# Kernel optimization log

Measured on AMD Instinct MI355X. Metric: run time of the kernel, lower is better.

The kernel has to match this reference:

```python
import jax, jax.numpy as jnp
import numpy as np

N_NODES = 50000
N_EDGES = 320000
D_IN = 256
D_OUT = 256


def setup_inputs() -> dict:
    key = jax.random.key(0)
    k1, k2, k3, k4, k5, k6, k7 = jax.random.split(key, 7)
    s = 1.0 / np.sqrt(D_IN)
    return {
        "node_features": jax.random.normal(k1, (N_NODES, D_IN), dtype=jnp.float32),
        "edge_index": jax.random.randint(k2, (2, N_EDGES), 0, N_NODES, dtype=jnp.int64),
        "w1": jax.random.uniform(k3, (D_OUT, D_IN), jnp.float32, -s, s),
        "w2": jax.random.uniform(k4, (D_OUT, D_IN), jnp.float32, -s, s),
        "w3": jax.random.uniform(k5, (D_OUT, D_IN), jnp.float32, -s, s),
        "b3": jax.random.uniform(k6, (D_OUT,), jnp.float32, -s, s),
    }


def reference(node_features, edge_index, w1, w2, w3, b3):
    # GraphSAGE-style conv: project, gather messages from senders,
    # scatter-sum at receivers, project, combine with self term.
    n = node_features.shape[0]
    proj = node_features @ w3.T + b3                 # [N, D_OUT]
    msgs = proj[edge_index[0]]                       # [E, D_OUT] gather senders
    agg = jax.ops.segment_sum(msgs, edge_index[1], num_segments=n)  # [N, D_OUT]
    out = node_features @ w1.T + agg @ w2.T          # [N, D_OUT]
    return out
```

## Files before the change

kernel.cpp:

```cpp
#include <hip/hip_runtime.h>

#define NN 50000
#define NPAD 50048
#define NE 320000
#define D 256
#define CAP 64
#define NCONV 6250

typedef __bf16 bf16x8 __attribute__((ext_vector_type(8)));
typedef float f32x4 __attribute__((ext_vector_type(4)));

__device__ __forceinline__ unsigned short f2bf(float f) {
    unsigned u = __builtin_bit_cast(unsigned, f);
    unsigned r = u + 0x7FFFu + ((u >> 16) & 1u);
    return (unsigned short)(r >> 16);
}
__device__ __forceinline__ float bflo(unsigned u) {
    return __builtin_bit_cast(float, u << 16);
}
__device__ __forceinline__ float bfhi(unsigned u) {
    return __builtin_bit_cast(float, u & 0xFFFF0000u);
}
__device__ __forceinline__ unsigned packbf(float lo, float hi) {
    return (unsigned)f2bf(lo) | ((unsigned)f2bf(hi) << 16);
}

__global__ __launch_bounds__(256) void prep_weights(
        const float* __restrict__ w1, const float* __restrict__ w2,
        const float* __restrict__ w3, const float* __restrict__ b3,
        unsigned short* __restrict__ WTT, float* __restrict__ bvec,
        int* __restrict__ cnt) {
    const int j = blockIdx.x;
    const int k = threadIdx.x;
    const int g = j * 256 + k;
    if (g < NN) cnt[g] = 0;
    __shared__ float w2row[D];
    __shared__ float red[D];
    w2row[k] = w2[j * D + k];
    __syncthreads();
    float acc = 0.f;
    #pragma unroll 8
    for (int o = 0; o < D; ++o) acc += w2row[o] * w3[o * D + k];
    WTT[(size_t)j * 512 + k]     = f2bf(w1[j * D + k]);
    WTT[(size_t)j * 512 + D + k] = f2bf(acc);
    red[k] = w2row[k] * b3[k];
    __syncthreads();
    for (int s = 128; s > 0; s >>= 1) {
        if (k < s) red[k] += red[k + s];
        __syncthreads();
    }
    if (k == 0) bvec[j] = red[0];
}

__global__ __launch_bounds__(256) void convert_and_csr(
        const float* __restrict__ x, unsigned short* __restrict__ xbf,
        const int* __restrict__ ei, int* __restrict__ csr, int* __restrict__ cnt) {
    const int b = blockIdx.x;
    if (b < NCONV) {
        const size_t i = ((size_t)b * 256 + threadIdx.x) * 8;
        const float4 a0 = *reinterpret_cast<const float4*>(x + i);
        const float4 a1 = *reinterpret_cast<const float4*>(x + i + 4);
        ushort4 o0 = {f2bf(a0.x), f2bf(a0.y), f2bf(a0.z), f2bf(a0.w)};
        ushort4 o1 = {f2bf(a1.x), f2bf(a1.y), f2bf(a1.z), f2bf(a1.w)};
        *reinterpret_cast<ushort4*>(xbf + i)     = o0;
        *reinterpret_cast<ushort4*>(xbf + i + 4) = o1;
    } else {
        const int e = (b - NCONV) * 256 + threadIdx.x;
        if (e < NE) {
            const int src = ei[e];
            const int dst = ei[NE + e];
            const int pos = atomicAdd(cnt + dst, 1);
            if (pos < CAP) csr[(size_t)dst * CAP + pos] = src;
        }
    }
}

__global__ __launch_bounds__(256) void agg_gather(
        const unsigned short* __restrict__ xbf, const int* __restrict__ csr,
        const int* __restrict__ cnt, unsigned short* __restrict__ aggbf) {
    const int node = blockIdx.x * 8 + (threadIdx.x >> 5);
    const int l32  = threadIdx.x & 31;
    if (node >= NN) return;
    int d = cnt[node]; if (d > CAP) d = CAP;
    const int* __restrict__ row = csr + (size_t)node * CAP;
    const int d32 = d < 32 ? d : 32;
    int myidx = 0;
    if (l32 < d32) myidx = row[l32];
    float a0 = 0.f, a1 = 0.f, a2 = 0.f, a3 = 0.f;
    float a4 = 0.f, a5 = 0.f, a6 = 0.f, a7 = 0.f;
    int i = 0;
    for (; i + 4 <= d32; i += 4) {
        const int s0 = __shfl(myidx, i,     32);
        const int s1 = __shfl(myidx, i + 1, 32);
        const int s2 = __shfl(myidx, i + 2, 32);
        const int s3 = __shfl(myidx, i + 3, 32);
        const uint4 p = *reinterpret_cast<const uint4*>(xbf + (size_t)s0 * D + l32 * 8);
        const uint4 q = *reinterpret_cast<const uint4*>(xbf + (size_t)s1 * D + l32 * 8);
        const uint4 u = *reinterpret_cast<const uint4*>(xbf + (size_t)s2 * D + l32 * 8);
        const uint4 v = *reinterpret_cast<const uint4*>(xbf + (size_t)s3 * D + l32 * 8);
        a0 += (bflo(p.x) + bflo(q.x)) + (bflo(u.x) + bflo(v.x));
        a1 += (bfhi(p.x) + bfhi(q.x)) + (bfhi(u.x) + bfhi(v.x));
        a2 += (bflo(p.y) + bflo(q.y)) + (bflo(u.y) + bflo(v.y));
        a3 += (bfhi(p.y) + bfhi(q.y)) + (bfhi(u.y) + bfhi(v.y));
        a4 += (bflo(p.z) + bflo(q.z)) + (bflo(u.z) + bflo(v.z));
        a5 += (bfhi(p.z) + bfhi(q.z)) + (bfhi(u.z) + bfhi(v.z));
        a6 += (bflo(p.w) + bflo(q.w)) + (bflo(u.w) + bflo(v.w));
        a7 += (bfhi(p.w) + bfhi(q.w)) + (bfhi(u.w) + bfhi(v.w));
    }
    for (; i < d32; ++i) {
        const int s = __shfl(myidx, i, 32);
        const uint4 p = *reinterpret_cast<const uint4*>(xbf + (size_t)s * D + l32 * 8);
        a0 += bflo(p.x); a1 += bfhi(p.x);
        a2 += bflo(p.y); a3 += bfhi(p.y);
        a4 += bflo(p.z); a5 += bfhi(p.z);
        a6 += bflo(p.w); a7 += bfhi(p.w);
    }
    for (; i < d; ++i) {
        const uint4 p = *reinterpret_cast<const uint4*>(xbf + (size_t)row[i] * D + l32 * 8);
        a0 += bflo(p.x); a1 += bfhi(p.x);
        a2 += bflo(p.y); a3 += bfhi(p.y);
        a4 += bflo(p.z); a5 += bfhi(p.z);
        a6 += bflo(p.w); a7 += bfhi(p.w);
    }
    uint4 o = {packbf(a0, a1), packbf(a2, a3), packbf(a4, a5), packbf(a6, a7)};
    *reinterpret_cast<uint4*>(aggbf + (size_t)node * D + l32 * 8) = o;
}

__global__ __launch_bounds__(256) void gemm_tiled(
        const unsigned short* __restrict__ xbf, const unsigned short* __restrict__ aggbf,
        const unsigned short* __restrict__ WTT, const float* __restrict__ bvec,
        const int* __restrict__ cnt, float* __restrict__ out) {
    __shared__ __align__(16) unsigned short ldsA[64 * 64];
    __shared__ __align__(16) unsigned short ldsB[128 * 64];

    const int tid  = threadIdx.x;
    const int w    = tid >> 6;
    const int lane = tid & 63;
    const int l16  = lane & 15;
    const int g4   = lane >> 4;
    const int wm   = w >> 1, wn = w & 1;
    const int gr0  = (blockIdx.x >> 1) * 64;
    const int nb0  = (blockIdx.x & 1) * 128;

    f32x4 acc[2][4];
    #pragma unroll
    for (int a = 0; a < 2; ++a)
        #pragma unroll
        for (int b = 0; b < 4; ++b) acc[a][b] = (f32x4)0.f;

    for (int kt = 0; kt < 8; ++kt) {
        if (kt) __syncthreads();
        {
            const unsigned short* __restrict__ srcA = (kt < 4) ? xbf : aggbf;
            const int kcA = (kt & 3) * 64;
            #pragma unroll
            for (int p = 0; p < 2; ++p) {
                const int idx = p * 256 + w * 64 + lane;
                const int r = idx >> 3, c = idx & 7;
                const int sw = (c ^ (r & 7)) << 3;
                const unsigned short* gp = srcA + ((size_t)(gr0 + r) << 8) + kcA + sw;
                unsigned short* lp = &ldsA[(p * 256 + w * 64) << 3];
                __builtin_amdgcn_global_load_lds(
                    (const __attribute__((address_space(1))) void*)(const void*)gp,
                    (__attribute__((address_space(3))) void*)(void*)lp, 16, 0, 0);
            }
            const int kcB = kt * 64;
            #pragma unroll
            for (int p = 0; p < 4; ++p) {
                const int idx = p * 256 + w * 64 + lane;
                const int r = idx >> 3, c = idx & 7;
                const int sw = (c ^ (r & 7)) << 3;
                const unsigned short* gp = WTT + ((size_t)(nb0 + r) << 9) + kcB + sw;
                unsigned short* lp = &ldsB[(p * 256 + w * 64) << 3];
                __builtin_amdgcn_global_load_lds(
                    (const __attribute__((address_space(1))) void*)(const void*)gp,
                    (__attribute__((address_space(3))) void*)(void*)lp, 16, 0, 0);
            }
        }
        __syncthreads();

        #pragma unroll
        for (int kh = 0; kh < 2; ++kh) {
            const int cb = kh * 4 + g4;
            bf16x8 af[2], bfr[4];
            #pragma unroll
            for (int f = 0; f < 2; ++f) {
                const int ra = wm * 32 + f * 16 + l16;
                af[f] = *reinterpret_cast<const bf16x8*>(
                    &ldsA[(ra * 8 + (cb ^ (ra & 7))) * 8]);
            }
            #pragma unroll
            for (int f = 0; f < 4; ++f) {
                const int rb = wn * 64 + f * 16 + l16;
                bfr[f] = *reinterpret_cast<const bf16x8*>(
                    &ldsB[(rb * 8 + (cb ^ (rb & 7))) * 8]);
            }
            #pragma unroll
            for (int fm = 0; fm < 2; ++fm)
                #pragma unroll
                for (int fn = 0; fn < 4; ++fn)
                    acc[fm][fn] = __builtin_amdgcn_mfma_f32_16x16x32_bf16(
                        af[fm], bfr[fn], acc[fm][fn], 0, 0, 0);
        }
    }

    const int col0 = nb0 + wn * 64 + l16;
    float bv[4];
    #pragma unroll
    for (int fn = 0; fn < 4; ++fn) bv[fn] = bvec[col0 + fn * 16];
    #pragma unroll
    for (int fm = 0; fm < 2; ++fm) {
        #pragma unroll
        for (int i = 0; i < 4; ++i) {
            const int row = gr0 + wm * 32 + fm * 16 + g4 * 4 + i;
            if (row < NN) {
                const float dg = (float)cnt[row];
                float* op = out + ((size_t)row << 8) + col0;
                #pragma unroll
                for (int fn = 0; fn < 4; ++fn)
                    op[fn * 16] = acc[fm][fn][i] + dg * bv[fn];
            }
        }
    }
}

extern "C" void kernel_launch(void* const* d_in, const int* in_sizes, int n_in,
                              void* d_out, int out_size, void* d_ws, size_t ws_size,
                              hipStream_t stream) {
    const float* x  = (const float*)d_in[0];
    const int*   ei = (const int*)d_in[1];
    const float* w1 = (const float*)d_in[2];
    const float* w2 = (const float*)d_in[3];
    const float* w3 = (const float*)d_in[4];
    const float* b3 = (const float*)d_in[5];
    float* out = (float*)d_out;

    unsigned short* xbf   = (unsigned short*)d_ws;
    unsigned short* aggbf = xbf + (size_t)NPAD * D;
    unsigned short* WTT   = aggbf + (size_t)NPAD * D;
    float* bvec = (float*)(WTT + (size_t)D * 512);
    int*   cnt  = (int*)(bvec + D);
    int*   csr  = cnt + NN;

    prep_weights<<<D, 256, 0, stream>>>(w1, w2, w3, b3, WTT, bvec, cnt);
    convert_and_csr<<<NCONV + (NE + 255) / 256, 256, 0, stream>>>(x, xbf, ei, csr, cnt);
    agg_gather<<<(NN + 7) / 8, 256, 0, stream>>>(xbf, csr, cnt, aggbf);
    gemm_tiled<<<(NPAD / 64) * 2, 256, 0, stream>>>(xbf, aggbf, WTT, bvec, cnt, out);
}
```

Baseline: 101.1 us.

## Reorder CSR blocks first, sort neighbor indices, XCD-remap GEMM tiles, stage epilogue through LDS

The combined convert/CSR kernel now puts the edge-scatter blocks first so the atomics start early. The gather kernel bitonic-sorts each node's first 32 neighbor indices across lanes so loads run in address order, and sorting also makes the summation order deterministic. The GEMM remaps workgroup IDs so consecutive tiles land on the same XCD for L2 locality. Its epilogue stages accumulators through LDS to emit coalesced float4 stores, at the cost of extra barriers and LDS traffic.

```diff
diff --git a/kernel.cpp b/kernel.cpp
--- a/kernel.cpp
+++ b/kernel.cpp
@@ -5,6 +5,7 @@
 #define NE 320000
 #define D 256
 #define CAP 64
+#define NCSR 1250
 #define NCONV 6250
 
 typedef __bf16 bf16x8 __attribute__((ext_vector_type(8)));
@@ -56,22 +57,22 @@
         const float* __restrict__ x, unsigned short* __restrict__ xbf,
         const int* __restrict__ ei, int* __restrict__ csr, int* __restrict__ cnt) {
     const int b = blockIdx.x;
-    if (b < NCONV) {
-        const size_t i = ((size_t)b * 256 + threadIdx.x) * 8;
+    if (b < NCSR) {
+        const int e = b * 256 + threadIdx.x;
+        if (e < NE) {
+            const int src = ei[e];
+            const int dst = ei[NE + e];
+            const int pos = atomicAdd(cnt + dst, 1);
+            if (pos < CAP) csr[(size_t)dst * CAP + pos] = src;
+        }
+    } else {
+        const size_t i = ((size_t)(b - NCSR) * 256 + threadIdx.x) * 8;
         const float4 a0 = *reinterpret_cast<const float4*>(x + i);
         const float4 a1 = *reinterpret_cast<const float4*>(x + i + 4);
         ushort4 o0 = {f2bf(a0.x), f2bf(a0.y), f2bf(a0.z), f2bf(a0.w)};
         ushort4 o1 = {f2bf(a1.x), f2bf(a1.y), f2bf(a1.z), f2bf(a1.w)};
         *reinterpret_cast<ushort4*>(xbf + i)     = o0;
         *reinterpret_cast<ushort4*>(xbf + i + 4) = o1;
-    } else {
-        const int e = (b - NCONV) * 256 + threadIdx.x;
-        if (e < NE) {
-            const int src = ei[e];
-            const int dst = ei[NE + e];
-            const int pos = atomicAdd(cnt + dst, 1);
-            if (pos < CAP) csr[(size_t)dst * CAP + pos] = src;
-        }
     }
 }
 
@@ -84,31 +85,42 @@
     int d = cnt[node]; if (d > CAP) d = CAP;
     const int* __restrict__ row = csr + (size_t)node * CAP;
     const int d32 = d < 32 ? d : 32;
-    int myidx = 0;
-    if (l32 < d32) myidx = row[l32];
+    int v = (l32 < d32) ? row[l32] : 0x7FFFFFFF;
+    #pragma unroll
+    for (int k = 2; k <= 32; k <<= 1) {
+        #pragma unroll
+        for (int j = k >> 1; j > 0; j >>= 1) {
+            const int o = __shfl_xor(v, j, 32);
+            const int lo = v < o ? v : o;
+            const int hi = v < o ? o : v;
+            const bool dir   = (l32 & k) == 0;
+            const bool lower = (l32 & j) == 0;
+            v = (dir == lower) ? lo : hi;
+        }
+    }
     float a0 = 0.f, a1 = 0.f, a2 = 0.f, a3 = 0.f;
     float a4 = 0.f, a5 = 0.f, a6 = 0.f, a7 = 0.f;
     int i = 0;
     for (; i + 4 <= d32; i += 4) {
-        const int s0 = __shfl(myidx, i,     32);
-        const int s1 = __shfl(myidx, i + 1, 32);
-        const int s2 = __shfl(myidx, i + 2, 32);
-        const int s3 = __shfl(myidx, i + 3, 32);
+        const int s0 = __shfl(v, i,     32);
+        const int s1 = __shfl(v, i + 1, 32);
+        const int s2 = __shfl(v, i + 2, 32);
+        const int s3 = __shfl(v, i + 3, 32);
         const uint4 p = *reinterpret_cast<const uint4*>(xbf + (size_t)s0 * D + l32 * 8);
         const uint4 q = *reinterpret_cast<const uint4*>(xbf + (size_t)s1 * D + l32 * 8);
         const uint4 u = *reinterpret_cast<const uint4*>(xbf + (size_t)s2 * D + l32 * 8);
-        const uint4 v = *reinterpret_cast<const uint4*>(xbf + (size_t)s3 * D + l32 * 8);
-        a0 += (bflo(p.x) + bflo(q.x)) + (bflo(u.x) + bflo(v.x));
-        a1 += (bfhi(p.x) + bfhi(q.x)) + (bfhi(u.x) + bfhi(v.x));
-        a2 += (bflo(p.y) + bflo(q.y)) + (bflo(u.y) + bflo(v.y));
-        a3 += (bfhi(p.y) + bfhi(q.y)) + (bfhi(u.y) + bfhi(v.y));
-        a4 += (bflo(p.z) + bflo(q.z)) + (bflo(u.z) + bflo(v.z));
-        a5 += (bfhi(p.z) + bfhi(q.z)) + (bfhi(u.z) + bfhi(v.z));
-        a6 += (bflo(p.w) + bflo(q.w)) + (bflo(u.w) + bflo(v.w));
-        a7 += (bfhi(p.w) + bfhi(q.w)) + (bfhi(u.w) + bfhi(v.w));
+        const uint4 t = *reinterpret_cast<const uint4*>(xbf + (size_t)s3 * D + l32 * 8);
+        a0 += (bflo(p.x) + bflo(q.x)) + (bflo(u.x) + bflo(t.x));
+        a1 += (bfhi(p.x) + bfhi(q.x)) + (bfhi(u.x) + bfhi(t.x));
+        a2 += (bflo(p.y) + bflo(q.y)) + (bflo(u.y) + bflo(t.y));
+        a3 += (bfhi(p.y) + bfhi(q.y)) + (bfhi(u.y) + bfhi(t.y));
+        a4 += (bflo(p.z) + bflo(q.z)) + (bflo(u.z) + bflo(t.z));
+        a5 += (bfhi(p.z) + bfhi(q.z)) + (bfhi(u.z) + bfhi(t.z));
+        a6 += (bflo(p.w) + bflo(q.w)) + (bflo(u.w) + bflo(t.w));
+        a7 += (bfhi(p.w) + bfhi(q.w)) + (bfhi(u.w) + bfhi(t.w));
     }
     for (; i < d32; ++i) {
-        const int s = __shfl(myidx, i, 32);
+        const int s = __shfl(v, i, 32);
         const uint4 p = *reinterpret_cast<const uint4*>(xbf + (size_t)s * D + l32 * 8);
         a0 += bflo(p.x); a1 += bfhi(p.x);
         a2 += bflo(p.y); a3 += bfhi(p.y);
@@ -130,8 +142,14 @@
         const unsigned short* __restrict__ xbf, const unsigned short* __restrict__ aggbf,
         const unsigned short* __restrict__ WTT, const float* __restrict__ bvec,
         const int* __restrict__ cnt, float* __restrict__ out) {
-    __shared__ __align__(16) unsigned short ldsA[64 * 64];
-    __shared__ __align__(16) unsigned short ldsB[128 * 64];
+    __shared__ __align__(16) unsigned char smem[24576];
+    unsigned short* ldsA = (unsigned short*)smem;
+    unsigned short* ldsB = (unsigned short*)(smem + 8192);
+
+    const int nwg = gridDim.x;
+    const int q   = nwg >> 3, r = nwg & 7;
+    const int xcd = blockIdx.x & 7, pos = blockIdx.x >> 3;
+    const int wg  = (xcd < r ? xcd * (q + 1) : r * (q + 1) + (xcd - r) * q) + pos;
 
     const int tid  = threadIdx.x;
     const int w    = tid >> 6;
@@ -139,8 +157,8 @@
     const int l16  = lane & 15;
     const int g4   = lane >> 4;
     const int wm   = w >> 1, wn = w & 1;
-    const int gr0  = (blockIdx.x >> 1) * 64;
-    const int nb0  = (blockIdx.x & 1) * 128;
+    const int gr0  = (wg >> 1) * 64;
+    const int nb0  = (wg & 1) * 128;
 
     f32x4 acc[2][4];
     #pragma unroll
@@ -156,10 +174,10 @@
             #pragma unroll
             for (int p = 0; p < 2; ++p) {
                 const int idx = p * 256 + w * 64 + lane;
-                const int r = idx >> 3, c = idx & 7;
-                const int sw = (c ^ (r & 7)) << 3;
-                const unsigned short* gp = srcA + ((size_t)(gr0 + r) << 8) + kcA + sw;
-                unsigned short* lp = &ldsA[(p * 256 + w * 64) << 3];
+                const int rr = idx >> 3, c = idx & 7;
+                const int sw = (c ^ (rr & 7)) << 3;
+                const unsigned short* gp = srcA + ((size_t)(gr0 + rr) << 8) + kcA + sw;
+                unsigned short* lp = ldsA + ((p * 256 + w * 64) << 3);
                 __builtin_amdgcn_global_load_lds(
                     (const __attribute__((address_space(1))) void*)(const void*)gp,
                     (__attribute__((address_space(3))) void*)(void*)lp, 16, 0, 0);
@@ -168,10 +186,10 @@
             #pragma unroll
             for (int p = 0; p < 4; ++p) {
                 const int idx = p * 256 + w * 64 + lane;
-                const int r = idx >> 3, c = idx & 7;
-                const int sw = (c ^ (r & 7)) << 3;
-                const unsigned short* gp = WTT + ((size_t)(nb0 + r) << 9) + kcB + sw;
-                unsigned short* lp = &ldsB[(p * 256 + w * 64) << 3];
+                const int rr = idx >> 3, c = idx & 7;
+                const int sw = (c ^ (rr & 7)) << 3;
+                const unsigned short* gp = WTT + ((size_t)(nb0 + rr) << 9) + kcB + sw;
+                unsigned short* lp = ldsB + ((p * 256 + w * 64) << 3);
                 __builtin_amdgcn_global_load_lds(
                     (const __attribute__((address_space(1))) void*)(const void*)gp,
                     (__attribute__((address_space(3))) void*)(void*)lp, 16, 0, 0);
@@ -187,13 +205,13 @@
             for (int f = 0; f < 2; ++f) {
                 const int ra = wm * 32 + f * 16 + l16;
                 af[f] = *reinterpret_cast<const bf16x8*>(
-                    &ldsA[(ra * 8 + (cb ^ (ra & 7))) * 8]);
+                    ldsA + (ra * 8 + (cb ^ (ra & 7))) * 8);
             }
             #pragma unroll
             for (int f = 0; f < 4; ++f) {
                 const int rb = wn * 64 + f * 16 + l16;
                 bfr[f] = *reinterpret_cast<const bf16x8*>(
-                    &ldsB[(rb * 8 + (cb ^ (rb & 7))) * 8]);
+                    ldsB + (rb * 8 + (cb ^ (rb & 7))) * 8);
             }
             #pragma unroll
             for (int fm = 0; fm < 2; ++fm)
@@ -204,21 +222,35 @@
         }
     }
 
-    const int col0 = nb0 + wn * 64 + l16;
-    float bv[4];
+    float* O = (float*)smem;
     #pragma unroll
-    for (int fn = 0; fn < 4; ++fn) bv[fn] = bvec[col0 + fn * 16];
-    #pragma unroll
-    for (int fm = 0; fm < 2; ++fm) {
-        #pragma unroll
-        for (int i = 0; i < 4; ++i) {
-            const int row = gr0 + wm * 32 + fm * 16 + g4 * 4 + i;
+    for (int half = 0; half < 2; ++half) {
+        __syncthreads();
+        if (wm == half) {
+            #pragma unroll
+            for (int fm = 0; fm < 2; ++fm)
+                #pragma unroll
+                for (int i = 0; i < 4; ++i) {
+                    const int lr = fm * 16 + g4 * 4 + i;
+                    float* po = O + lr * 132 + wn * 64 + l16;
+                    #pragma unroll
+                    for (int fn = 0; fn < 4; ++fn) po[fn * 16] = acc[fm][fn][i];
+                }
+        }
+        __syncthreads();
+        #pragma unroll
+        for (int p = 0; p < 4; ++p) {
+            const int id = tid + p * 256;
+            const int rr = id >> 5;
+            const int c4 = (id & 31) << 2;
+            const int row = gr0 + half * 32 + rr;
             if (row < NN) {
                 const float dg = (float)cnt[row];
-                float* op = out + ((size_t)row << 8) + col0;
-                #pragma unroll
-                for (int fn = 0; fn < 4; ++fn)
-                    op[fn * 16] = acc[fm][fn][i] + dg * bv[fn];
+                const float4 bv = *reinterpret_cast<const float4*>(bvec + nb0 + c4);
+                float4 vv = *reinterpret_cast<const float4*>(O + rr * 132 + c4);
+                vv.x += dg * bv.x; vv.y += dg * bv.y;
+                vv.z += dg * bv.z; vv.w += dg * bv.w;
+                *reinterpret_cast<float4*>(out + ((size_t)row << 8) + nb0 + c4) = vv;
             }
         }
     }
@@ -243,7 +275,7 @@
     int*   csr  = cnt + NN;
 
     prep_weights<<<D, 256, 0, stream>>>(w1, w2, w3, b3, WTT, bvec, cnt);
-    convert_and_csr<<<NCONV + (NE + 255) / 256, 256, 0, stream>>>(x, xbf, ei, csr, cnt);
+    convert_and_csr<<<NCSR + NCONV, 256, 0, stream>>>(x, xbf, ei, csr, cnt);
     agg_gather<<<(NN + 7) / 8, 256, 0, stream>>>(xbf, csr, cnt, aggbf);
     gemm_tiled<<<(NPAD / 64) * 2, 256, 0, stream>>>(xbf, aggbf, WTT, bvec, cnt, out);
 }
```

New measurement: 97.13 us (median of 2 runs). 1.04x faster.
